# Performance work log

Measured on AMD Instinct MI355X. Metric: run time of the kernel, lower is better.

## Reference

```python
import jax, jax.numpy as jnp
import numpy as np
import math

S, B, D = 2048, 2, 1024
H = 16
DH = D // H
WIN = 256
DIL = 1


def setup_inputs() -> dict:
    key = jax.random.key(0)
    ks = jax.random.split(key, 10)
    std = 1.0 / math.sqrt(D)
    return {
        "x": jax.random.normal(ks[0], (S, B, D), jnp.float32),
        "beta": jax.random.normal(ks[1], (H,), jnp.float32) * 0.02,
        "Wq": jax.random.normal(ks[2], (D, D), jnp.float32) * std,
        "bq": jnp.zeros((D,), jnp.float32),
        "Wk": jax.random.normal(ks[3], (D, D), jnp.float32) * std,
        "bk": jnp.zeros((D,), jnp.float32),
        "Wv": jax.random.normal(ks[4], (D, D), jnp.float32) * std,
        "bv": jnp.zeros((D,), jnp.float32),
        "Wo": jax.random.normal(ks[5], (D, D), jnp.float32) * std,
        "bo": jnp.zeros((D,), jnp.float32),
    }


def _split_heads(t):
    # (S, B, D) -> (B*H, S, DH), matching rearrange 's b (h d) -> (b h) s d'
    return t.reshape(S, B, H, DH).transpose(1, 2, 0, 3).reshape(B * H, S, DH)


def reference(x, beta, Wq, bq, Wk, bk, Wv, bv, Wo, bo):
    q = _split_heads(x @ Wq + bq)
    k = _split_heads(x @ Wk + bk)
    v = _split_heads(x @ Wv + bv)

    # per-head learnable temperature: q / (sqrt(d_head) * exp(beta))
    beta_exp = jnp.tile(jnp.exp(beta), B)  # (B*H,), head index = z % H
    q = q / (jnp.sqrt(jnp.asarray(DH, x.dtype)) * beta_exp)[:, None, None]

    # causal dilated windowed mask
    idx = jnp.arange(S)
    diff = idx[:, None] - idx[None, :]
    allowed = (diff >= 0) & (diff <= DIL * (WIN - 1)) & (diff % DIL == 0)
    mask = jnp.where(allowed, jnp.asarray(0.0, x.dtype), jnp.asarray(-jnp.inf, x.dtype))

    scores = jnp.einsum('zqd,zkd->zqk', q, k) + mask[None]
    # attention sink: extra zero-logit column absorbing probability mass
    scores = jnp.concatenate([scores, jnp.zeros((B * H, S, 1), scores.dtype)], axis=-1)
    attn = jax.nn.softmax(scores, axis=-1)[..., :-1]

    out = jnp.einsum('zqk,zkd->zqd', attn, v)
    # (B*H, S, DH) -> (S, B, D)
    out = out.reshape(B, H, S, DH).transpose(2, 0, 1, 3).reshape(S, B, D)
    return out @ Wo + bo
```

## Files before the change

kernel.cpp:

```cpp
#include <hip/hip_runtime.h>
#include <math.h>

#define S_LEN  2048
#define BATCH  2
#define DM     1024
#define NHEAD  16
#define DHEAD  64
#define WIN    256
#define MROWS  4096

#define KP   72
#define PPAD 68

typedef __attribute__((ext_vector_type(8))) short bf16x8;
typedef __attribute__((ext_vector_type(4))) float f32x4;

__device__ __forceinline__ float b2f(unsigned short u) {
    union { unsigned int i; float f; } x; x.i = ((unsigned int)u) << 16; return x.f;
}
__device__ __forceinline__ unsigned short f2b(float f) {
    unsigned int u = __float_as_uint(f);
    return (unsigned short)((u + 0x7fffu + ((u >> 16) & 1u)) >> 16);
}
__device__ __forceinline__ void gld16(const void* g, void* l) {
    __builtin_amdgcn_global_load_lds(
        (const __attribute__((address_space(1))) void*)g,
        (__attribute__((address_space(3))) void*)l, 16, 0, 0);
}
__device__ __forceinline__ bf16x8 pack8(float4 a, float4 b) {
    bf16x8 r;
    r[0] = (short)f2b(a.x); r[1] = (short)f2b(a.y);
    r[2] = (short)f2b(a.z); r[3] = (short)f2b(a.w);
    r[4] = (short)f2b(b.x); r[5] = (short)f2b(b.y);
    r[6] = (short)f2b(b.z); r[7] = (short)f2b(b.w);
    return r;
}

__global__ __launch_bounds__(256)
void cvtx(const float* __restrict__ x, unsigned short* __restrict__ xb)
{
    const int i = (blockIdx.x * 256 + threadIdx.x) * 4;
    float4 f = *(const float4*)(x + i);
    ushort4 o; o.x = f2b(f.x); o.y = f2b(f.y); o.z = f2b(f.z); o.w = f2b(f.w);
    *(ushort4*)(xb + i) = o;
}

__global__ __launch_bounds__(256)
void twcvt(const float* __restrict__ W, unsigned short* __restrict__ WT)
{
    __shared__ float t32[32][33];
    const int bx = blockIdx.x * 32;
    const int by = blockIdx.y * 32;
    const int c  = threadIdx.x & 31;
    const int r0 = threadIdx.x >> 5;
#pragma unroll
    for (int p = 0; p < 4; ++p)
        t32[r0 + 8 * p][c] = W[(size_t)(by + r0 + 8 * p) * DM + bx + c];
    __syncthreads();
#pragma unroll
    for (int p = 0; p < 4; ++p)
        WT[(size_t)(bx + r0 + 8 * p) * DM + by + c] = f2b(t32[c][r0 + 8 * p]);
}

__global__ __launch_bounds__(256, 2)
void gemm_mfma(const unsigned short* __restrict__ A,
               const unsigned short* __restrict__ BT,
               const float* __restrict__ bias,
               const float* __restrict__ beta,
               float* __restrict__ Cf,
               unsigned short* __restrict__ Cb,
               int mode)
{
    __shared__ unsigned short As[128 * 32];
    __shared__ unsigned short Bs[64 * 32];

    const int t  = threadIdx.x;
    const int wv = t >> 6, ln = t & 63;
    const int rowBase = blockIdx.y * 128;
    const int colBase = blockIdx.x * 64;

    const int lr = ln >> 2;
    const int lk = (ln & 3) * 8;
    const int m16 = ln & 15;
    const int q8  = (ln >> 4) * 8;
    const int wr = wv >> 1, wc = wv & 1;

    const unsigned short* ga = A  + (size_t)(rowBase + wv * 32 + lr) * DM + lk;
    const unsigned short* gb = BT + (size_t)(colBase + wv * 16 + lr) * DM + lk;
    unsigned short* la0 = As + wv * 1024;
    unsigned short* la1 = la0 + 512;
    unsigned short* lb  = Bs + wv * 512;

    f32x4 acc[4][2];
#pragma unroll
    for (int u = 0; u < 4; ++u)
#pragma unroll
        for (int v = 0; v < 2; ++v)
            acc[u][v] = (f32x4){0.f, 0.f, 0.f, 0.f};

    for (int kb = 0; kb < DM; kb += 32) {
        gld16(ga + kb, la0);
        gld16(ga + 16 * DM + kb, la1);
        gld16(gb + kb, lb);
        __syncthreads();

        bf16x8 af[4], bfr[2];
#pragma unroll
        for (int u = 0; u < 4; ++u)
            af[u] = *(const bf16x8*)&As[(wr * 64 + u * 16 + m16) * 32 + q8];
#pragma unroll
        for (int v = 0; v < 2; ++v)
            bfr[v] = *(const bf16x8*)&Bs[(wc * 32 + v * 16 + m16) * 32 + q8];
#pragma unroll
        for (int u = 0; u < 4; ++u)
#pragma unroll
            for (int v = 0; v < 2; ++v)
                acc[u][v] = __builtin_amdgcn_mfma_f32_16x16x32_bf16(
                    af[u], bfr[v], acc[u][v], 0, 0, 0);
        __syncthreads();
    }

    const int roww = rowBase + wr * 64;
    const int colw = colBase + wc * 32;
    const int q4 = (ln >> 4) * 4;
    if (mode == 0) {
#pragma unroll
        for (int u = 0; u < 4; ++u)
#pragma unroll
            for (int v = 0; v < 2; ++v) {
                const int col = colw + v * 16 + m16;
                const float bi = bias[col];
#pragma unroll
                for (int r = 0; r < 4; ++r) {
                    const int row = roww + u * 16 + q4 + r;
                    Cf[(size_t)row * DM + col] = acc[u][v][r] + bi;
                }
            }
    } else if (mode == 3) {
#pragma unroll
        for (int u = 0; u < 4; ++u)
#pragma unroll
            for (int v = 0; v < 2; ++v) {
                const int col = colw + v * 16 + m16;
                const int s = col >> 1, bb = col & 1;
#pragma unroll
                for (int r = 0; r < 4; ++r) {
                    const int row = roww + u * 16 + q4 + r;
                    const int hh = row >> 6, dh = row & 63;
                    const int z  = bb * NHEAD + hh;
                    Cb[((size_t)z * DHEAD + dh) * S_LEN + s] =
                        f2b(acc[u][v][r] + bias[row]);
                }
            }
    } else {
        const int h = colBase >> 6;
        const float scale = (mode == 1) ? 0.125f * __expf(-beta[h]) : 1.0f;
#pragma unroll
        for (int u = 0; u < 4; ++u)
#pragma unroll
            for (int v = 0; v < 2; ++v) {
                const int col = colw + v * 16 + m16;
                const int dh  = col & 63;
                const float bi = bias[col];
#pragma unroll
                for (int r = 0; r < 4; ++r) {
                    const int row = roww + u * 16 + q4 + r;
                    const int s = row >> 1, bb = row & 1;
                    const int z = bb * NHEAD + h;
                    Cb[((size_t)z * S_LEN + s) * DHEAD + dh] =
                        f2b((acc[u][v][r] + bi) * scale);
                }
            }
    }
}

__global__ __launch_bounds__(256, 4)
void attn_mfma(const unsigned short* __restrict__ q,
               const unsigned short* __restrict__ k,
               const unsigned short* __restrict__ vt,
               unsigned short* __restrict__ ao)
{
    __shared__ unsigned short Ks[64 * KP];
    __shared__ unsigned short Vs[64 * KP];
    __shared__ float Ps[64][PPAD];

    const int t   = threadIdx.x;
    const int wv  = t >> 6, ln = t & 63;
    const int m16 = ln & 15, g = ln >> 4;
    const int z   = blockIdx.y;
    const int q0  = blockIdx.x * 64;
    const size_t zbase = (size_t)z * S_LEN * DHEAD;

    const unsigned short* qrow = q + zbase + (size_t)(q0 + wv * 16 + m16) * DHEAD;
    bf16x8 qf0 = *(const bf16x8*)(qrow + g * 8);
    bf16x8 qf1 = *(const bf16x8*)(qrow + 32 + g * 8);

    f32x4 oacc[4];
#pragma unroll
    for (int v4 = 0; v4 < 4; ++v4) oacc[v4] = (f32x4){0.f, 0.f, 0.f, 0.f};
    float mr[4], lr[4];
#pragma unroll
    for (int r = 0; r < 4; ++r) { mr[r] = 0.f; lr[r] = 1.f; }

    for (int c = 0; c < 5; ++c) {
        const int kb = q0 - 256 + c * 64;
        if (kb < 0) continue;
        __syncthreads();

#pragma unroll
        for (int i = 0; i < 2; ++i) {
            const int id  = t + 256 * i;
            const int row = id >> 3;
            const int co  = (id & 7) * 8;
            *(bf16x8*)&Ks[row * KP + co] =
                *(const bf16x8*)(k + zbase + (size_t)(kb + row) * DHEAD + co);
            *(bf16x8*)&Vs[row * KP + co] =
                *(const bf16x8*)(vt + ((size_t)z * DHEAD + row) * S_LEN + kb + co);
        }
        __syncthreads();

        f32x4 sacc[4];
#pragma unroll
        for (int v4 = 0; v4 < 4; ++v4) {
            sacc[v4] = (f32x4){0.f, 0.f, 0.f, 0.f};
            bf16x8 kf0 = *(const bf16x8*)&Ks[(v4 * 16 + m16) * KP + g * 8];
            sacc[v4] = __builtin_amdgcn_mfma_f32_16x16x32_bf16(qf0, kf0, sacc[v4], 0, 0, 0);
            bf16x8 kf1 = *(const bf16x8*)&Ks[(v4 * 16 + m16) * KP + 32 + g * 8];
            sacc[v4] = __builtin_amdgcn_mfma_f32_16x16x32_bf16(qf1, kf1, sacc[v4], 0, 0, 0);
        }

        const bool mhi = (c == 4), mlo = (c == 0);
#pragma unroll
        for (int r = 0; r < 4; ++r) {
            const int ig = q0 + wv * 16 + g * 4 + r;
            float sv[4];
            float smax = -1e30f;
#pragma unroll
            for (int v4 = 0; v4 < 4; ++v4) {
                const int jg = kb + v4 * 16 + m16;
                float x = sacc[v4][r];
                const bool valid = (!mhi || jg <= ig) && (!mlo || jg >= ig - (WIN - 1));
                x = valid ? x : -1e30f;
                sv[v4] = x;
                smax = fmaxf(smax, x);
            }
#pragma unroll
            for (int off = 1; off < 16; off <<= 1)
                smax = fmaxf(smax, __shfl_xor(smax, off, 64));
            const float mnew  = fmaxf(mr[r], smax);
            const float alpha = __expf(mr[r] - mnew);
            float rsum = 0.f;
#pragma unroll
            for (int v4 = 0; v4 < 4; ++v4) {
                const float pp = __expf(sv[v4] - mnew);
                Ps[wv * 16 + g * 4 + r][v4 * 16 + m16] = pp;
                rsum += pp;
            }
#pragma unroll
            for (int off = 1; off < 16; off <<= 1)
                rsum += __shfl_xor(rsum, off, 64);
            lr[r] = lr[r] * alpha + rsum;
            mr[r] = mnew;
#pragma unroll
            for (int v4 = 0; v4 < 4; ++v4) oacc[v4][r] *= alpha;
        }
        __syncthreads();

        const float* prow = &Ps[wv * 16 + m16][0];
        bf16x8 pf0 = pack8(*(const float4*)(prow + g * 8),
                           *(const float4*)(prow + g * 8 + 4));
        bf16x8 pf1 = pack8(*(const float4*)(prow + 32 + g * 8),
                           *(const float4*)(prow + 32 + g * 8 + 4));
#pragma unroll
        for (int v4 = 0; v4 < 4; ++v4) {
            bf16x8 vf0 = *(const bf16x8*)&Vs[(v4 * 16 + m16) * KP + g * 8];
            oacc[v4] = __builtin_amdgcn_mfma_f32_16x16x32_bf16(pf0, vf0, oacc[v4], 0, 0, 0);
            bf16x8 vf1 = *(const bf16x8*)&Vs[(v4 * 16 + m16) * KP + 32 + g * 8];
            oacc[v4] = __builtin_amdgcn_mfma_f32_16x16x32_bf16(pf1, vf1, oacc[v4], 0, 0, 0);
        }
    }

    const int bb = z >> 4, h = z & 15;
#pragma unroll
    for (int r = 0; r < 4; ++r) {
        const int ig  = q0 + wv * 16 + g * 4 + r;
        const float inv = 1.f / lr[r];
#pragma unroll
        for (int v4 = 0; v4 < 4; ++v4)
            ao[(size_t)(ig * BATCH + bb) * DM + h * DHEAD + v4 * 16 + m16] =
                f2b(oacc[v4][r] * inv);
    }
}

extern "C" void kernel_launch(void* const* d_in, const int* in_sizes, int n_in,
                              void* d_out, int out_size, void* d_ws, size_t ws_size,
                              hipStream_t stream)
{
    const float* x    = (const float*)d_in[0];
    const float* beta = (const float*)d_in[1];
    const float* Wq   = (const float*)d_in[2];
    const float* bq   = (const float*)d_in[3];
    const float* Wk   = (const float*)d_in[4];
    const float* bk   = (const float*)d_in[5];
    const float* Wv   = (const float*)d_in[6];
    const float* bv   = (const float*)d_in[7];
    const float* Wo   = (const float*)d_in[8];
    const float* bo   = (const float*)d_in[9];
    float* out = (float*)d_out;

    unsigned short* w = (unsigned short*)d_ws;
    const size_t seg = (size_t)MROWS * DM;
    unsigned short* qb  = w;
    unsigned short* kbf = w + seg;
    unsigned short* vtb = w + 2 * seg;
    unsigned short* ab  = w + 3 * seg;
    unsigned short* xb  = w + 4 * seg;
    unsigned short* wtq = w + 5 * seg;
    unsigned short* wtk = wtq + (size_t)DM * DM;
    unsigned short* wtv = wtk + (size_t)DM * DM;
    unsigned short* wto = wtv + (size_t)DM * DM;

    cvtx<<<4096, 256, 0, stream>>>(x, xb);
    dim3 tg(32, 32);
    twcvt<<<tg, 256, 0, stream>>>(Wq, wtq);
    twcvt<<<tg, 256, 0, stream>>>(Wk, wtk);
    twcvt<<<tg, 256, 0, stream>>>(Wv, wtv);
    twcvt<<<tg, 256, 0, stream>>>(Wo, wto);

    dim3 gg(DM / 64, MROWS / 128);
    gemm_mfma<<<gg, 256, 0, stream>>>(xb, wtq, bq, beta, nullptr, qb,  1);
    gemm_mfma<<<gg, 256, 0, stream>>>(xb, wtk, bk, beta, nullptr, kbf, 2);
    dim3 gv(MROWS / 64, DM / 128);
    gemm_mfma<<<gv, 256, 0, stream>>>(wtv, xb, bv, beta, nullptr, vtb, 3);

    attn_mfma<<<dim3(S_LEN / 64, BATCH * NHEAD), 256, 0, stream>>>(qb, kbf, vtb, ab);

    gemm_mfma<<<gg, 256, 0, stream>>>(ab, wto, bo, beta, out, nullptr, 0);
}
```

Before: 206.2 us.

## Enlarge GEMM tiles to 128x128, swizzle LDS, fuse QK projection and weight transposes

GEMM block tiles grow from 128x64 to 128x128, with 16 accumulators per wave and an XOR swizzle on the LDS layout to avoid bank conflicts. The Q and K projections run as one GEMM over a concatenated 2048-wide weight, which relies on wtq and wtk being contiguous in the workspace. The four weight-transpose launches are merged into a single launch using a z-grid. The aim is more data reuse per tile and fewer launches, at the cost of higher register pressure and the removal of the occupancy hint.

```diff
diff --git a/kernel.cpp b/kernel.cpp
--- a/kernel.cpp
+++ b/kernel.cpp
@@ -15,9 +15,6 @@
 typedef __attribute__((ext_vector_type(8))) short bf16x8;
 typedef __attribute__((ext_vector_type(4))) float f32x4;
 
-__device__ __forceinline__ float b2f(unsigned short u) {
-    union { unsigned int i; float f; } x; x.i = ((unsigned int)u) << 16; return x.f;
-}
 __device__ __forceinline__ unsigned short f2b(float f) {
     unsigned int u = __float_as_uint(f);
     return (unsigned short)((u + 0x7fffu + ((u >> 16) & 1u)) >> 16);
@@ -46,8 +43,15 @@
 }
 
 __global__ __launch_bounds__(256)
-void twcvt(const float* __restrict__ W, unsigned short* __restrict__ WT)
-{
+void twcvt4(const float* __restrict__ W0, const float* __restrict__ W1,
+            const float* __restrict__ W2, const float* __restrict__ W3,
+            unsigned short* __restrict__ T0, unsigned short* __restrict__ T1,
+            unsigned short* __restrict__ T2, unsigned short* __restrict__ T3)
+{
+    const int zz = blockIdx.z;
+    const float* W = (zz == 0) ? W0 : (zz == 1) ? W1 : (zz == 2) ? W2 : W3;
+    unsigned short* WT = (zz == 0) ? T0 : (zz == 1) ? T1 : (zz == 2) ? T2 : T3;
+
     __shared__ float t32[32][33];
     const int bx = blockIdx.x * 32;
     const int by = blockIdx.y * 32;
@@ -62,113 +66,116 @@
         WT[(size_t)(bx + r0 + 8 * p) * DM + by + c] = f2b(t32[c][r0 + 8 * p]);
 }
 
-__global__ __launch_bounds__(256, 2)
+__global__ __launch_bounds__(256)
 void gemm_mfma(const unsigned short* __restrict__ A,
                const unsigned short* __restrict__ BT,
                const float* __restrict__ bias,
+               const float* __restrict__ bias2,
                const float* __restrict__ beta,
                float* __restrict__ Cf,
                unsigned short* __restrict__ Cb,
                int mode)
 {
     __shared__ unsigned short As[128 * 32];
-    __shared__ unsigned short Bs[64 * 32];
+    __shared__ unsigned short Bs[128 * 32];
 
     const int t  = threadIdx.x;
     const int wv = t >> 6, ln = t & 63;
     const int rowBase = blockIdx.y * 128;
-    const int colBase = blockIdx.x * 64;
+    const int colBase = blockIdx.x * 128;
+
+    const int m16 = ln & 15, g = ln >> 4;
+    const int wr = wv >> 1, wc = wv & 1;
+    const int swz = m16 & 3;
 
     const int lr = ln >> 2;
-    const int lk = (ln & 3) * 8;
-    const int m16 = ln & 15;
-    const int q8  = (ln >> 4) * 8;
-    const int wr = wv >> 1, wc = wv & 1;
-
-    const unsigned short* ga = A  + (size_t)(rowBase + wv * 32 + lr) * DM + lk;
-    const unsigned short* gb = BT + (size_t)(colBase + wv * 16 + lr) * DM + lk;
-    unsigned short* la0 = As + wv * 1024;
-    unsigned short* la1 = la0 + 512;
-    unsigned short* lb  = Bs + wv * 512;
-
-    f32x4 acc[4][2];
+    const int lq = (ln & 3) ^ (lr & 3);
+    const unsigned short* ga = A  + (size_t)(rowBase + wv * 16 + lr) * DM + lq * 8;
+    const unsigned short* gb = BT + (size_t)(colBase + wv * 16 + lr) * DM + lq * 8;
+    unsigned short* la0 = As + wv * 512;
+    unsigned short* la1 = la0 + 2048;
+    unsigned short* lb0 = Bs + wv * 512;
+    unsigned short* lb1 = lb0 + 2048;
+
+    f32x4 acc[4][4];
 #pragma unroll
     for (int u = 0; u < 4; ++u)
 #pragma unroll
-        for (int v = 0; v < 2; ++v)
+        for (int v = 0; v < 4; ++v)
             acc[u][v] = (f32x4){0.f, 0.f, 0.f, 0.f};
 
     for (int kb = 0; kb < DM; kb += 32) {
         gld16(ga + kb, la0);
-        gld16(ga + 16 * DM + kb, la1);
-        gld16(gb + kb, lb);
-        __syncthreads();
-
-        bf16x8 af[4], bfr[2];
+        gld16(ga + (size_t)64 * DM + kb, la1);
+        gld16(gb + kb, lb0);
+        gld16(gb + (size_t)64 * DM + kb, lb1);
+        __syncthreads();
+
+        bf16x8 af[4], bfr[4];
 #pragma unroll
         for (int u = 0; u < 4; ++u)
-            af[u] = *(const bf16x8*)&As[(wr * 64 + u * 16 + m16) * 32 + q8];
-#pragma unroll
-        for (int v = 0; v < 2; ++v)
-            bfr[v] = *(const bf16x8*)&Bs[(wc * 32 + v * 16 + m16) * 32 + q8];
+            af[u] = *(const bf16x8*)&As[(wr * 64 + u * 16 + m16) * 32 + ((g ^ swz) * 8)];
+#pragma unroll
+        for (int v = 0; v < 4; ++v)
+            bfr[v] = *(const bf16x8*)&Bs[(wc * 64 + v * 16 + m16) * 32 + ((g ^ swz) * 8)];
 #pragma unroll
         for (int u = 0; u < 4; ++u)
 #pragma unroll
-            for (int v = 0; v < 2; ++v)
+            for (int v = 0; v < 4; ++v)
                 acc[u][v] = __builtin_amdgcn_mfma_f32_16x16x32_bf16(
                     af[u], bfr[v], acc[u][v], 0, 0, 0);
         __syncthreads();
     }
 
-    const int roww = rowBase + wr * 64;
-    const int colw = colBase + wc * 32;
-    const int q4 = (ln >> 4) * 4;
+    const int q4 = g * 4;
     if (mode == 0) {
 #pragma unroll
-        for (int u = 0; u < 4; ++u)
-#pragma unroll
-            for (int v = 0; v < 2; ++v) {
-                const int col = colw + v * 16 + m16;
-                const float bi = bias[col];
+        for (int v = 0; v < 4; ++v) {
+            const int col = colBase + wc * 64 + v * 16 + m16;
+            const float bi = bias[col];
+#pragma unroll
+            for (int u = 0; u < 4; ++u)
 #pragma unroll
                 for (int r = 0; r < 4; ++r) {
-                    const int row = roww + u * 16 + q4 + r;
+                    const int row = rowBase + wr * 64 + u * 16 + q4 + r;
                     Cf[(size_t)row * DM + col] = acc[u][v][r] + bi;
                 }
-            }
-    } else if (mode == 3) {
-#pragma unroll
-        for (int u = 0; u < 4; ++u)
-#pragma unroll
-            for (int v = 0; v < 2; ++v) {
-                const int col = colw + v * 16 + m16;
-                const int s = col >> 1, bb = col & 1;
+        }
+    } else if (mode == 1) {
+#pragma unroll
+        for (int v = 0; v < 4; ++v) {
+            const int col  = colBase + wc * 64 + v * 16 + m16;
+            const bool isq = (col < DM);
+            const int h    = (col >> 6) & (NHEAD - 1);
+            const int dh   = col & 63;
+            const float bi = isq ? bias[col] : bias2[col - DM];
+            const float sc = isq ? 0.125f * __expf(-beta[h]) : 1.0f;
+            unsigned short* base = Cb + (isq ? 0 : (size_t)MROWS * DM);
+#pragma unroll
+            for (int u = 0; u < 4; ++u)
 #pragma unroll
                 for (int r = 0; r < 4; ++r) {
-                    const int row = roww + u * 16 + q4 + r;
-                    const int hh = row >> 6, dh = row & 63;
-                    const int z  = bb * NHEAD + hh;
-                    Cb[((size_t)z * DHEAD + dh) * S_LEN + s] =
-                        f2b(acc[u][v][r] + bias[row]);
-                }
-            }
-    } else {
-        const int h = colBase >> 6;
-        const float scale = (mode == 1) ? 0.125f * __expf(-beta[h]) : 1.0f;
-#pragma unroll
-        for (int u = 0; u < 4; ++u)
-#pragma unroll
-            for (int v = 0; v < 2; ++v) {
-                const int col = colw + v * 16 + m16;
-                const int dh  = col & 63;
-                const float bi = bias[col];
-#pragma unroll
-                for (int r = 0; r < 4; ++r) {
-                    const int row = roww + u * 16 + q4 + r;
+                    const int row = rowBase + wr * 64 + u * 16 + q4 + r;
                     const int s = row >> 1, bb = row & 1;
                     const int z = bb * NHEAD + h;
-                    Cb[((size_t)z * S_LEN + s) * DHEAD + dh] =
-                        f2b((acc[u][v][r] + bi) * scale);
+                    base[((size_t)z * S_LEN + s) * DHEAD + dh] =
+                        f2b((acc[u][v][r] + bi) * sc);
+                }
+        }
+    } else {
+#pragma unroll
+        for (int u = 0; u < 4; ++u)
+#pragma unroll
+            for (int r = 0; r < 4; ++r) {
+                const int row = rowBase + wr * 64 + u * 16 + q4 + r;
+                const int hh = row >> 6, dh = row & 63;
+                const float bi = bias[row];
+#pragma unroll
+                for (int v = 0; v < 4; ++v) {
+                    const int col = colBase + wc * 64 + v * 16 + m16;
+                    const int s = col >> 1, bb = col & 1;
+                    Cb[((size_t)(bb * NHEAD + hh) * DHEAD + dh) * S_LEN + s] =
+                        f2b(acc[u][v][r] + bi);
                 }
             }
     }
@@ -321,19 +328,15 @@
     unsigned short* wto = wtv + (size_t)DM * DM;
 
     cvtx<<<4096, 256, 0, stream>>>(x, xb);
-    dim3 tg(32, 32);
-    twcvt<<<tg, 256, 0, stream>>>(Wq, wtq);
-    twcvt<<<tg, 256, 0, stream>>>(Wk, wtk);
-    twcvt<<<tg, 256, 0, stream>>>(Wv, wtv);
-    twcvt<<<tg, 256, 0, stream>>>(Wo, wto);
-
-    dim3 gg(DM / 64, MROWS / 128);
-    gemm_mfma<<<gg, 256, 0, stream>>>(xb, wtq, bq, beta, nullptr, qb,  1);
-    gemm_mfma<<<gg, 256, 0, stream>>>(xb, wtk, bk, beta, nullptr, kbf, 2);
-    dim3 gv(MROWS / 64, DM / 128);
-    gemm_mfma<<<gv, 256, 0, stream>>>(wtv, xb, bv, beta, nullptr, vtb, 3);
+    twcvt4<<<dim3(32, 32, 4), 256, 0, stream>>>(Wq, Wk, Wv, Wo, wtq, wtk, wtv, wto);
+
+    gemm_mfma<<<dim3(2048 / 128, MROWS / 128), 256, 0, stream>>>(
+        xb, wtq, bq, bk, beta, nullptr, qb, 1);
+    gemm_mfma<<<dim3(MROWS / 128, DM / 128), 256, 0, stream>>>(
+        wtv, xb, bv, nullptr, beta, nullptr, vtb, 3);
 
     attn_mfma<<<dim3(S_LEN / 64, BATCH * NHEAD), 256, 0, stream>>>(qb, kbf, vtb, ab);
 
-    gemm_mfma<<<gg, 256, 0, stream>>>(ab, wto, bo, beta, out, nullptr, 0);
-}
+    gemm_mfma<<<dim3(DM / 128, MROWS / 128), 256, 0, stream>>>(
+        ab, wto, bo, nullptr, beta, out, nullptr, 0);
+}
```

Result: faster. 194.3 us (-5.8%).
